# Kernel optimization log

Hardware: AMD Instinct MI355X
Metric: run time of the kernel (lower is better)

Reference implementation:

```python
import jax, jax.numpy as jnp
import numpy as np

N_NODES = 50000
N_GRAPHS = 128
HEADS = 10
F_XD = 78


def _linear(x, W, b):
    return x @ W + b


def _conv1d(x, w, b):
    # x: [B, Cin, L], w: [Cout, Cin, K]
    y = jax.lax.conv_general_dilated(x, w, (1,), 'VALID',
                                     dimension_numbers=('NCH', 'OIH', 'NCH'))
    return y + b[None, :, None]


def _add_self_loops(src, dst, n):
    loop = jnp.arange(n, dtype=src.dtype)
    return jnp.concatenate([src, loop]), jnp.concatenate([dst, loop])


def _gat_conv(x, src, dst, W, att_src, att_dst, b, n):
    # PyG GATConv, concat heads, self-loops, negative_slope=0.2
    h = (x @ W).reshape(n, HEADS, F_XD)               # [N,H,F]
    a_s = jnp.sum(h * att_src[None], axis=-1)          # [N,H]
    a_d = jnp.sum(h * att_dst[None], axis=-1)          # [N,H]
    e = jax.nn.leaky_relu(a_s[src] + a_d[dst], 0.2)    # [E,H]
    m = jax.ops.segment_max(e, dst, num_segments=n)    # [N,H]
    m = jnp.where(jnp.isfinite(m), m, 0.0)
    ex = jnp.exp(e - m[dst])
    s = jax.ops.segment_sum(ex, dst, num_segments=n)
    alpha = ex / (s[dst] + 1e-16)                      # [E,H]
    out = jax.ops.segment_sum(h[src] * alpha[:, :, None], dst, num_segments=n)
    return out.reshape(n, HEADS * F_XD) + b


def _gcn_conv(x, src, dst, W, b, n):
    # PyG GCNConv: self-loops + symmetric normalization
    h = x @ W                                          # [N,C]
    ones = jnp.ones(src.shape[0], dtype=h.dtype)
    deg = jax.ops.segment_sum(ones, dst, num_segments=n)
    dinv = jnp.where(deg > 0, jax.lax.rsqrt(deg), 0.0)
    norm = dinv[src] * dinv[dst]                       # [E]
    out = jax.ops.segment_sum(h[src] * norm[:, None], dst, num_segments=n)
    return out + b


def _forward(x, edge_index, batch, target1, target2, params):
    p = params
    n = x.shape[0]
    src0, dst0 = edge_index[0], edge_index[1]
    src, dst = _add_self_loops(src0, dst0, n)

    h = jax.nn.relu(_gat_conv(x, src, dst, p['W_gat'], p['att_src'], p['att_dst'], p['b_gat'], n))
    h = jax.nn.relu(_gcn_conv(h, src, dst, p['W_gcn'], p['b_gcn'], n))

    # global max + mean pool per graph
    cnt = jax.ops.segment_sum(jnp.ones(n, dtype=h.dtype), batch, num_segments=N_GRAPHS)
    gmx = jax.ops.segment_max(h, batch, num_segments=N_GRAPHS)
    gmx = jnp.where(cnt[:, None] > 0, gmx, 0.0)
    gav = jax.ops.segment_sum(h, batch, num_segments=N_GRAPHS) / jnp.maximum(cnt, 1.0)[:, None]
    g = jnp.concatenate([gmx, gav], axis=1)            # [B,1560]

    g = jax.nn.relu(_linear(g, p['W_fcg1'], p['b_fcg1']))  # dropout = identity (eval)
    g = _linear(g, p['W_fcg2'], p['b_fcg2'])               # [B,128]

    # protein branch 2: embedding + conv1d over embed dim
    emb = p['emb'][target2]                            # [B,1000,128]
    xt2 = _conv1d(emb, p['Wc2'], p['bc2'])             # [B,32,121]
    xt2 = _linear(xt2.reshape(xt2.shape[0], 32 * 121), p['W_fc2xt'], p['b_fc2xt'])

    # protein branch 1: conv1d on raw float features
    xt1 = _conv1d(target1, p['Wc1'], p['bc1'])         # [B,32,17]
    xt1 = _linear(xt1.reshape(xt1.shape[0], 544), p['W_fc1xt'], p['b_fc1xt'])

    xc = jnp.concatenate([g, xt1, xt2], axis=1)        # [B,384]
    xc = jax.nn.relu(_linear(xc, p['W_fc1'], p['b_fc1']))
    xc = jax.nn.relu(_linear(xc, p['W_fc2'], p['b_fc2']))
    return _linear(xc, p['W_out'], p['b_out'])         # [B,1]


def setup_inputs() -> dict:
    key = jax.random.key(0)
    ks = jax.random.split(key, 32)

    def w(k, shape, fan_in):
        return jax.random.normal(k, shape, dtype=jnp.float32) * (1.0 / np.sqrt(fan_in))

    inp = {}
    inp['x'] = jax.random.normal(ks[0], (N_NODES, F_XD), dtype=jnp.float32)
    inp['edge_index'] = jax.random.randint(ks[1], (2, 150000), 0, N_NODES, dtype=jnp.int64) if jax.config.jax_enable_x64 else jax.random.randint(ks[1], (2, 150000), 0, N_NODES).astype(jnp.int32)
    inp['batch'] = jnp.sort(jax.random.randint(ks[2], (N_NODES,), 0, N_GRAPHS)).astype(jnp.int32)
    inp['target1'] = jax.random.normal(ks[3], (N_GRAPHS, 20, 24), dtype=jnp.float32)
    inp['target2'] = jax.random.randint(ks[4], (N_GRAPHS, 1000), 0, 26).astype(jnp.int32)

    inp['W_gat'] = w(ks[5], (F_XD, HEADS * F_XD), F_XD)
    inp['att_src'] = w(ks[6], (HEADS, F_XD), F_XD)
    inp['att_dst'] = w(ks[7], (HEADS, F_XD), F_XD)
    inp['b_gat'] = jnp.zeros((HEADS * F_XD,), jnp.float32)
    inp['W_gcn'] = w(ks[8], (780, 780), 780)
    inp['b_gcn'] = jnp.zeros((780,), jnp.float32)
    inp['W_fcg1'] = w(ks[9], (1560, 1500), 1560)
    inp['b_fcg1'] = jnp.zeros((1500,), jnp.float32)
    inp['W_fcg2'] = w(ks[10], (1500, 128), 1500)
    inp['b_fcg2'] = jnp.zeros((128,), jnp.float32)
    inp['emb'] = jax.random.normal(ks[11], (26, 128), dtype=jnp.float32)
    inp['Wc2'] = w(ks[12], (32, 1000, 8), 1000 * 8)
    inp['bc2'] = jnp.zeros((32,), jnp.float32)
    inp['W_fc2xt'] = w(ks[13], (32 * 121, 128), 32 * 121)
    inp['b_fc2xt'] = jnp.zeros((128,), jnp.float32)
    inp['Wc1'] = w(ks[14], (32, 20, 8), 20 * 8)
    inp['bc1'] = jnp.zeros((32,), jnp.float32)
    inp['W_fc1xt'] = w(ks[15], (544, 128), 544)
    inp['b_fc1xt'] = jnp.zeros((128,), jnp.float32)
    inp['W_fc1'] = w(ks[16], (384, 1024), 384)
    inp['b_fc1'] = jnp.zeros((1024,), jnp.float32)
    inp['W_fc2'] = w(ks[17], (1024, 512), 1024)
    inp['b_fc2'] = jnp.zeros((512,), jnp.float32)
    inp['W_out'] = w(ks[18], (512, 1), 512)
    inp['b_out'] = jnp.zeros((1,), jnp.float32)
    return inp


def reference(x, edge_index, batch, target1, target2,
              W_gat, att_src, att_dst, b_gat, W_gcn, b_gcn,
              W_fcg1, b_fcg1, W_fcg2, b_fcg2, emb, Wc2, bc2,
              W_fc2xt, b_fc2xt, Wc1, bc1, W_fc1xt, b_fc1xt,
              W_fc1, b_fc1, W_fc2, b_fc2, W_out, b_out):
    params = dict(W_gat=W_gat, att_src=att_src, att_dst=att_dst, b_gat=b_gat,
                  W_gcn=W_gcn, b_gcn=b_gcn, W_fcg1=W_fcg1, b_fcg1=b_fcg1,
                  W_fcg2=W_fcg2, b_fcg2=b_fcg2, emb=emb, Wc2=Wc2, bc2=bc2,
                  W_fc2xt=W_fc2xt, b_fc2xt=b_fc2xt, Wc1=Wc1, bc1=bc1,
                  W_fc1xt=W_fc1xt, b_fc1xt=b_fc1xt, W_fc1=W_fc1, b_fc1=b_fc1,
                  W_fc2=W_fc2, b_fc2=b_fc2, W_out=W_out, b_out=b_out)
    return _forward(x, edge_index, batch, target1, target2, params)
```

## Files before the change

kernel.cpp:

```cpp
#include <hip/hip_runtime.h>
#include <cstdio>
#include <cstdint>

#define CDIV(a,b) (((a)+(b)-1)/(b))

static const int N   = 50000;
static const int NE0 = 150000;
static const int NE  = 200000;
static const int H   = 10;
static const int F   = 78;
static const int C   = 780;
static const int G   = 128;
static const int KP_GAT = 96;
static const int XAGG_LD = 960;
static const int CP1 = 800;
static const int CP1A = 832;
static const int CP2 = 784;
static const int POOL_SPLIT = 8;
static const int BM_SPLIT = 4;

typedef __attribute__((ext_vector_type(8))) short bf16x8;
typedef __attribute__((ext_vector_type(4))) float f32x4;
typedef __attribute__((ext_vector_type(8))) unsigned short us8;

__device__ __forceinline__ float bf2f(unsigned short u) {
    return __uint_as_float(((unsigned int)u) << 16);
}
__device__ __forceinline__ unsigned short f2bf(float f) {
    unsigned int u = __float_as_uint(f);
    u = (u + 0x7fff + ((u >> 16) & 1)) >> 16;
    return (unsigned short)u;
}

__device__ __forceinline__ void async16(const unsigned short* g, unsigned short* l) {
    __builtin_amdgcn_global_load_lds(
        (const __attribute__((address_space(1))) unsigned int*)g,
        (__attribute__((address_space(3))) unsigned int*)l, 16, 0, 0);
}

__global__ __launch_bounds__(512)
void gemm_mfma_256(const unsigned short* __restrict__ A,
                   const unsigned short* __restrict__ Bt,
                   unsigned short* __restrict__ Cb,
                   const float* __restrict__ bias, int relu,
                   int M, int Nn, int kSteps, int lda, int ldb, int ldc, int nct)
{
    __shared__ unsigned short As[256][64];
    __shared__ unsigned short Bs[128][64];
    const int tid  = threadIdx.x;
    const int lane = tid & 63;
    const int wave = tid >> 6;
    const int wm = (wave >> 1) * 64;
    const int wn = (wave & 1) * 64;

    const int nwg = gridDim.x;
    const int q8 = nwg >> 3, r8 = nwg & 7;
    const int xcd = blockIdx.x & 7, sub = blockIdx.x >> 3;
    const int wg = (xcd < r8) ? xcd * (q8 + 1) + sub
                              : r8 * (q8 + 1) + (xcd - r8) * q8 + sub;
    const int bm = (wg / nct) * 256, bn = (wg % nct) * 128;

    f32x4 acc[4][4] = {};

    const int mrow = lane & 15, quad = lane >> 4;
    const int srow = lane >> 3;
    const int segoff = ((lane & 7) ^ (lane >> 3)) * 8;

    const unsigned short* gA[4];
    unsigned short* lA[4];
#pragma unroll
    for (int c = 0; c < 4; c++) {
        int r = c * 64 + wave * 8 + srow;
        gA[c] = A + (size_t)min(bm + r, M - 1) * lda + segoff;
        lA[c] = &As[c * 64 + wave * 8][0];
    }
    const unsigned short* gB[2];
    unsigned short* lB[2];
#pragma unroll
    for (int c = 0; c < 2; c++) {
        int r = c * 64 + wave * 8 + srow;
        gB[c] = Bt + (size_t)min(bn + r, Nn - 1) * ldb + segoff;
        lB[c] = &Bs[c * 64 + wave * 8][0];
    }

    for (int ks = 0; ks < kSteps; ks++) {
        const int k0 = ks * 64;
#pragma unroll
        for (int c = 0; c < 4; c++) async16(gA[c] + k0, lA[c]);
#pragma unroll
        for (int c = 0; c < 2; c++) async16(gB[c] + k0, lB[c]);
        __syncthreads();
#pragma unroll
        for (int kk = 0; kk < 2; kk++) {
            bf16x8 af[4], bfr[4];
#pragma unroll
            for (int i = 0; i < 4; i++) {
                int ra = wm + i * 16 + mrow;
                af[i]  = *(const bf16x8*)&As[ra][(((kk * 4 + quad) ^ (ra & 7))) * 8];
                int rb = wn + i * 16 + mrow;
                bfr[i] = *(const bf16x8*)&Bs[rb][(((kk * 4 + quad) ^ (rb & 7))) * 8];
            }
#pragma unroll
            for (int i = 0; i < 4; i++)
#pragma unroll
                for (int j = 0; j < 4; j++)
                    acc[i][j] = __builtin_amdgcn_mfma_f32_16x16x32_bf16(af[i], bfr[j], acc[i][j], 0, 0, 0);
        }
        __syncthreads();
    }

#pragma unroll
    for (int i = 0; i < 4; i++) {
#pragma unroll
        for (int j = 0; j < 4; j++) {
            int col = bn + wn + j * 16 + mrow;
            if (col >= Nn) continue;
            float bv = bias ? bias[col] : 0.f;
#pragma unroll
            for (int r = 0; r < 4; r++) {
                int row = bm + wm + i * 16 + quad * 4 + r;
                if (row >= M) continue;
                float v = acc[i][j][r] + bv;
                if (relu) v = fmaxf(v, 0.f);
                Cb[(size_t)row * ldc + col] = f2bf(v);
            }
        }
    }
}

__global__ __launch_bounds__(256)
void gemm_gat(const unsigned short* __restrict__ A,
              const unsigned short* __restrict__ Bt,
              const float* __restrict__ bias,
              unsigned short* __restrict__ Cb)
{
    __shared__ unsigned short As[128][32];
    __shared__ unsigned short Bs[128][32];
    const int tid  = threadIdx.x;
    const int lane = tid & 63;
    const int wave = tid >> 6;
    const int wm = (wave >> 1) * 64, wn = (wave & 1) * 64;
    const int h = blockIdx.y;

    const int nwg = gridDim.x;
    const int q8 = nwg >> 3, r8 = nwg & 7;
    const int xcd = blockIdx.x & 7, sub = blockIdx.x >> 3;
    const int wg = (xcd < r8) ? xcd * (q8 + 1) + sub
                              : r8 * (q8 + 1) + (xcd - r8) * q8 + sub;
    const int bm = wg * 128;

    f32x4 acc[4][4] = {};

    const int mrow = lane & 15, quad = lane >> 4;
    const int subr = lane >> 2;
    const int segp = ((lane & 3) ^ ((lane >> 3) & 3)) * 8;
    const int segr = (quad ^ ((mrow >> 1) & 3)) * 8;

    const unsigned short* gA0 = A + (size_t)min(bm + wave * 16 + subr,      N - 1) * XAGG_LD + h * KP_GAT + segp;
    const unsigned short* gA1 = A + (size_t)min(bm + 64 + wave * 16 + subr, N - 1) * XAGG_LD + h * KP_GAT + segp;
    const unsigned short* gB0 = Bt + (size_t)(h * 80 + min(wave * 16 + subr,      79)) * KP_GAT + segp;
    const unsigned short* gB1 = Bt + (size_t)(h * 80 + min(64 + wave * 16 + subr, 79)) * KP_GAT + segp;
    unsigned short* lA0 = &As[wave * 16][0];
    unsigned short* lA1 = &As[64 + wave * 16][0];
    unsigned short* lB0 = &Bs[wave * 16][0];
    unsigned short* lB1 = &Bs[64 + wave * 16][0];

#pragma unroll
    for (int ks = 0; ks < 3; ks++) {
        const int k0 = ks * 32;
        async16(gA0 + k0, lA0);
        async16(gA1 + k0, lA1);
        async16(gB0 + k0, lB0);
        async16(gB1 + k0, lB1);
        __syncthreads();
        bf16x8 af[4], bfr[4];
#pragma unroll
        for (int i = 0; i < 4; i++) {
            af[i]  = *(const bf16x8*)&As[wm + i * 16 + mrow][segr];
            bfr[i] = *(const bf16x8*)&Bs[wn + i * 16 + mrow][segr];
        }
#pragma unroll
        for (int i = 0; i < 4; i++)
#pragma unroll
            for (int j = 0; j < 4; j++)
                acc[i][j] = __builtin_amdgcn_mfma_f32_16x16x32_bf16(af[i], bfr[j], acc[i][j], 0, 0, 0);
        __syncthreads();
    }

#pragma unroll
    for (int i = 0; i < 4; i++) {
#pragma unroll
        for (int j = 0; j < 4; j++) {
            int cl = wn + j * 16 + mrow;
            if (cl >= 80) continue;
            float bv = bias[h * 80 + cl];
#pragma unroll
            for (int r = 0; r < 4; r++) {
                int row = bm + wm + i * 16 + quad * 4 + r;
                if (row >= N) continue;
                float v = fmaxf(acc[i][j][r] + bv, 0.f);
                Cb[(size_t)row * CP1A + h * 80 + cl] = f2bf(v);
            }
        }
    }
}

__global__ __launch_bounds__(256)
void gemm_mfma_sk(const unsigned short* __restrict__ A,
                  const unsigned short* __restrict__ Bt,
                  float* __restrict__ Cp,
                  int M, int Nn, int kSteps, int lda, int ldb, int nct)
{
    __shared__ unsigned short As[128][32];
    __shared__ unsigned short Bs[128][32];
    const int tid  = threadIdx.x;
    const int lane = tid & 63;
    const int wave = tid >> 6;
    const int wm = (wave >> 1) * 64, wn = (wave & 1) * 64;
    const int bm = (blockIdx.x / nct) * 128, bn = (blockIdx.x % nct) * 128;

    const int split = blockIdx.y, KS = gridDim.y;
    const int per = CDIV(kSteps, KS);
    const int kb = split * per;
    const int ke = min(kb + per, kSteps);

    f32x4 acc[4][4] = {};

    const int mrow = lane & 15, quad = lane >> 4;
    const int subr = lane >> 2;
    const int segp = ((lane & 3) ^ ((lane >> 3) & 3)) * 8;
    const int segr = (quad ^ ((mrow >> 1) & 3)) * 8;

    const unsigned short* gA0 = A  + (size_t)min(bm + wave * 16 + subr,      M - 1)  * lda + segp;
    const unsigned short* gA1 = A  + (size_t)min(bm + 64 + wave * 16 + subr, M - 1)  * lda + segp;
    const unsigned short* gB0 = Bt + (size_t)min(bn + wave * 16 + subr,      Nn - 1) * ldb + segp;
    const unsigned short* gB1 = Bt + (size_t)min(bn + 64 + wave * 16 + subr, Nn - 1) * ldb + segp;
    unsigned short* lA0 = &As[wave * 16][0];
    unsigned short* lA1 = &As[64 + wave * 16][0];
    unsigned short* lB0 = &Bs[wave * 16][0];
    unsigned short* lB1 = &Bs[64 + wave * 16][0];

    for (int ks = kb; ks < ke; ks++) {
        const int k0 = ks * 32;
        async16(gA0 + k0, lA0);
        async16(gA1 + k0, lA1);
        async16(gB0 + k0, lB0);
        async16(gB1 + k0, lB1);
        __syncthreads();
        bf16x8 af[4], bfr[4];
#pragma unroll
        for (int i = 0; i < 4; i++) {
            af[i]  = *(const bf16x8*)&As[wm + i * 16 + mrow][segr];
            bfr[i] = *(const bf16x8*)&Bs[wn + i * 16 + mrow][segr];
        }
#pragma unroll
        for (int i = 0; i < 4; i++)
#pragma unroll
            for (int j = 0; j < 4; j++)
                acc[i][j] = __builtin_amdgcn_mfma_f32_16x16x32_bf16(af[i], bfr[j], acc[i][j], 0, 0, 0);
        __syncthreads();
    }

    float* Cs = Cp + (size_t)split * M * Nn;
#pragma unroll
    for (int i = 0; i < 4; i++) {
#pragma unroll
        for (int j = 0; j < 4; j++) {
            int col = bn + wn + j * 16 + mrow;
            if (col >= Nn) continue;
#pragma unroll
            for (int r = 0; r < 4; r++) {
                int row = bm + wm + i * 16 + quad * 4 + r;
                if (row >= M) continue;
                Cs[(size_t)row * Nn + col] = acc[i][j][r];
            }
        }
    }
}

__global__ void k_sk_reduce(const float* __restrict__ Cp, int KS, int M, int Nn,
                            const float* __restrict__ bias, int relu,
                            unsigned short* __restrict__ Cb, int ldc)
{
    int idx = blockIdx.x * blockDim.x + threadIdx.x;
    if (idx >= M * Nn) return;
    int row = idx / Nn, col = idx % Nn;
    float v = bias ? bias[col] : 0.f;
    for (int s = 0; s < KS; s++) v += Cp[((size_t)s * M + row) * Nn + col];
    if (relu) v = fmaxf(v, 0.f);
    Cb[(size_t)row * ldc + col] = f2bf(v);
}

__global__ void k_fc_out(const unsigned short* __restrict__ f2, const float* __restrict__ W,
                         const float* __restrict__ b, float* __restrict__ out)
{
    int g = blockIdx.x, lane = threadIdx.x;
    float acc = 0.f;
    for (int k = lane; k < 512; k += 64) acc += bf2f(f2[g * 512 + k]) * W[k];
#pragma unroll
    for (int off = 32; off > 0; off >>= 1) acc += __shfl_down(acc, off, 64);
    if (lane == 0) out[g] = acc + b[0];
}

__global__ void k_cast_pad_x(const float* __restrict__ x, unsigned short* __restrict__ xb)
{
    int idx = blockIdx.x * blockDim.x + threadIdx.x;
    if (idx >= N * KP_GAT) return;
    int n = idx / KP_GAT, k = idx % KP_GAT;
    float v = (k < F) ? x[(size_t)n * F + k] : 0.f;
    xb[idx] = f2bf(v);
}

__global__ void k_transpose_cast_t(const float* __restrict__ W, unsigned short* __restrict__ Wt,
                                   int K, int Nn, int Kpad)
{
    __shared__ float tile[32][33];
    int k0 = blockIdx.x * 32, n0 = blockIdx.y * 32;
    int tx = threadIdx.x, ty = threadIdx.y;
    for (int r = ty; r < 32; r += 8) {
        int k = k0 + r, n = n0 + tx;
        tile[r][tx] = (k < K && n < Nn) ? W[(size_t)k * Nn + n] : 0.f;
    }
    __syncthreads();
    for (int r = ty; r < 32; r += 8) {
        int n = n0 + r, k = k0 + tx;
        if (n < Nn && k < Kpad) Wt[(size_t)n * Kpad + k] = f2bf(tile[tx][r]);
    }
}

__global__ void k_build_Wgat_t(const float* __restrict__ W_gat, unsigned short* __restrict__ Wt)
{
    int idx = blockIdx.x * blockDim.x + threadIdx.x;
    if (idx >= KP_GAT * CP1) return;
    int k = idx / CP1, n = idx % CP1;
    int h = n / 80, f = n % 80;
    float v = (k < F && f < F) ? W_gat[(size_t)k * C + h * F + f] : 0.f;
    Wt[(size_t)n * KP_GAT + k] = f2bf(v);
}

__global__ void k_build_bgat(const float* __restrict__ b_gat, float* __restrict__ bp)
{
    int i = blockIdx.x * blockDim.x + threadIdx.x;
    if (i >= CP1) return;
    int h = i / 80, f = i % 80;
    bp[i] = (f < F) ? b_gat[h * F + f] : 0.f;
}

__global__ void k_build_Wgcn_t(const float* __restrict__ W_gcn, unsigned short* __restrict__ Wt)
{
    int idx = blockIdx.x * blockDim.x + threadIdx.x;
    if (idx >= C * CP2) return;
    int ko = idx / CP2, n = idx % CP2;
    int h = ko / F, f = ko % F;
    float v = (n < C) ? W_gcn[(size_t)ko * C + n] : 0.f;
    Wt[(size_t)n * CP1A + h * 80 + f] = f2bf(v);
}

__global__ void k_Vsd(const float* __restrict__ W_gat, const float* __restrict__ att_src,
                      const float* __restrict__ att_dst, float* __restrict__ V_s,
                      float* __restrict__ V_d)
{
    int idx = blockIdx.x * blockDim.x + threadIdx.x;
    if (idx >= F * H) return;
    int k = idx / H, h = idx % H;
    const float* wr = W_gat + (size_t)k * C + h * F;
    const float* as = att_src + h * F;
    const float* ad = att_dst + h * F;
    float s = 0.f, d = 0.f;
    for (int f = 0; f < F; f++) { float w = wr[f]; s += w * as[f]; d += w * ad[f]; }
    V_s[idx] = s; V_d[idx] = d;
}

__global__ void k_ascores(const float* __restrict__ x, const float* __restrict__ V_s,
                          const float* __restrict__ V_d, float* __restrict__ a_s,
                          float* __restrict__ a_d)
{
    __shared__ float Vs[F * H], Vd[F * H];
    int t = threadIdx.x;
    for (int i = t; i < F * H; i += 256) { Vs[i] = V_s[i]; Vd[i] = V_d[i]; }
    __syncthreads();
    int n = blockIdx.x * 256 + t;
    if (n >= N) return;
    const float* xr = x + (size_t)n * F;
    float accs[H] = {}, accd[H] = {};
    for (int k = 0; k < F; k++) {
        float xv = xr[k];
        const float* vs = &Vs[k * H];
        const float* vd = &Vd[k * H];
#pragma unroll
        for (int h = 0; h < H; h++) { accs[h] += xv * vs[h]; accd[h] += xv * vd[h]; }
    }
    for (int h = 0; h < H; h++) { a_s[n * H + h] = accs[h]; a_d[n * H + h] = accd[h]; }
}

__global__ void count_deg(const int* __restrict__ ei, int* __restrict__ deg)
{
    int e = blockIdx.x * blockDim.x + threadIdx.x;
    if (e >= NE) return;
    int d = (e < NE0) ? ei[NE0 + e] : (e - NE0);
    atomicAdd(&deg[d], 1);
}

__global__ void scan_int(const int* __restrict__ cnt, int* __restrict__ row_start, int n)
{
    __shared__ int partial[1024];
    int tid = threadIdx.x;
    int per = CDIV(n, 1024);
    int start = tid * per, end = min(start + per, n);
    int sum = 0;
    for (int i = start; i < end; i++) sum += cnt[i];
    partial[tid] = sum;
    __syncthreads();
    for (int off = 1; off < 1024; off *= 2) {
        int v = (tid >= off) ? partial[tid - off] : 0;
        __syncthreads();
        partial[tid] += v;
        __syncthreads();
    }
    int base = (tid > 0) ? partial[tid - 1] : 0;
    for (int i = start; i < end; i++) { row_start[i] = base; base += cnt[i]; }
    if (tid == 1023) row_start[n] = base;
}

__global__ void fill_csr_ev(const int* __restrict__ ei, const int* __restrict__ row_start,
                            int* __restrict__ fill_cnt, int* __restrict__ srcs,
                            const float* __restrict__ a_s, const float* __restrict__ a_d,
                            float* __restrict__ evb)
{
    int e = blockIdx.x * blockDim.x + threadIdx.x;
    if (e >= NE) return;
    int sr = (e < NE0) ? ei[e] : (e - NE0);
    int d  = (e < NE0) ? ei[NE0 + e] : (e - NE0);
    int pos = row_start[d] + atomicAdd(&fill_cnt[d], 1);
    srcs[pos] = sr;
    const float* as = a_s + sr * H;
    const float* ad = a_d + d * H;
    float* ev = evb + (size_t)pos * H;
#pragma unroll
    for (int h = 0; h < H; h++) {
        float v = as[h] + ad[h];
        ev[h] = (v > 0.f) ? v : 0.2f * v;
    }
}

__global__ void k_gstart(const int* __restrict__ batch, int* __restrict__ gstart)
{
    int g = blockIdx.x * blockDim.x + threadIdx.x;
    if (g > G) return;
    int lo = 0, hi = N;
    while (lo < hi) {
        int mid = (lo + hi) >> 1;
        if (batch[mid] < g) lo = mid + 1; else hi = mid;
    }
    gstart[g] = lo;
}

__global__ void k_softmax_alpha(const int* __restrict__ row_start, float* __restrict__ evb)
{
    int idx = blockIdx.x * blockDim.x + threadIdx.x;
    if (idx >= N * H) return;
    int n = idx / H, h = idx % H;
    int rs = row_start[n], re = row_start[n + 1];
    float m = -INFINITY, s = 0.f;
    for (int i = rs; i < re; i++) {
        float ev = evb[(size_t)i * H + h];
        if (ev <= m) {
            s += expf(ev - m);
        } else {
            s = s * expf(m - ev) + 1.f;
            m = ev;
        }
    }
    float inv = 1.f / (s + 1e-16f);
    for (int i = rs; i < re; i++) {
        float ev = evb[(size_t)i * H + h];
        evb[(size_t)i * H + h] = expf(ev - m) * inv;
    }
}

__global__ __launch_bounds__(128)
void gat_agg_x(const unsigned short* __restrict__ xb, const float* __restrict__ alpha,
               const int* __restrict__ srcs, const int* __restrict__ row_start,
               unsigned short* __restrict__ xagg)
{
    int n = blockIdx.x;
    int f = threadIdx.x;
    if (f >= KP_GAT) return;
    int rs = row_start[n], re = row_start[n + 1];
    float acc[H] = {};
    int i = rs;
    for (; i + 1 < re; i += 2) {
        int sr0 = srcs[i], sr1 = srcs[i + 1];
        float xv0 = bf2f(xb[(size_t)sr0 * KP_GAT + f]);
        float xv1 = bf2f(xb[(size_t)sr1 * KP_GAT + f]);
        const float* al0 = alpha + (size_t)i * H;
        const float* al1 = alpha + (size_t)(i + 1) * H;
#pragma unroll
        for (int h = 0; h < H; h++) acc[h] += al0[h] * xv0 + al1[h] * xv1;
    }
    if (i < re) {
        int sr = srcs[i];
        float xv = bf2f(xb[(size_t)sr * KP_GAT + f]);
        const float* al = alpha + (size_t)i * H;
#pragma unroll
        for (int h = 0; h < H; h++) acc[h] += al[h] * xv;
    }
#pragma unroll
    for (int h = 0; h < H; h++)
        xagg[(size_t)n * XAGG_LD + h * KP_GAT + f] = f2bf(acc[h]);
}

__global__ void k_zero_tail(unsigned short* __restrict__ gat_out)
{
    int idx = blockIdx.x * blockDim.x + threadIdx.x;
    if (idx >= N * 32) return;
    int n = idx / 32, c = idx % 32;
    gat_out[(size_t)n * CP1A + CP1 + c] = 0;
}

__global__ void k_dinv(const int* __restrict__ deg, float* __restrict__ dinv)
{
    int n = blockIdx.x * blockDim.x + threadIdx.x;
    if (n >= N) return;
    int d = deg[n];
    dinv[n] = (d > 0) ? 1.f / sqrtf((float)d) : 0.f;
}

__global__ __launch_bounds__(128)
void gcn_agg(const unsigned short* __restrict__ h2, const float* __restrict__ dinv,
             const int* __restrict__ srcs, const int* __restrict__ row_start,
             const float* __restrict__ b_gcn, unsigned short* __restrict__ out)
{
    int n = blockIdx.x;
    int c = threadIdx.x * 8;
    if (c >= CP2) return;
    float dn = dinv[n];
    int rs = row_start[n], re = row_start[n + 1];
    float acc[8] = {};
    int i = rs;
    for (; i + 1 < re; i += 2) {
        int sr0 = srcs[i], sr1 = srcs[i + 1];
        float d0 = dinv[sr0], d1 = dinv[sr1];
        us8 v0 = *(const us8*)&h2[(size_t)sr0 * CP2 + c];
        us8 v1 = *(const us8*)&h2[(size_t)sr1 * CP2 + c];
#pragma unroll
        for (int j = 0; j < 8; j++) acc[j] += d0 * bf2f(v0[j]) + d1 * bf2f(v1[j]);
    }
    if (i < re) {
        int sr = srcs[i];
        float d = dinv[sr];
        us8 v = *(const us8*)&h2[(size_t)sr * CP2 + c];
#pragma unroll
        for (int j = 0; j < 8; j++) acc[j] += d * bf2f(v[j]);
    }
    us8 o;
#pragma unroll
    for (int j = 0; j < 8; j++) {
        int col = c + j;
        float r = (col < C) ? fmaxf(acc[j] * dn + b_gcn[col], 0.f) : 0.f;
        o[j] = f2bf(r);
    }
    *(us8*)&out[(size_t)n * CP2 + c] = o;
}

__global__ __launch_bounds__(128)
void k_pool(const unsigned short* __restrict__ hh, const int* __restrict__ gstart,
            float* __restrict__ gfeat)
{
    int g = blockIdx.x;
    int c = threadIdx.x * 8;
    if (c >= CP2) return;
    int s0 = gstart[g], e0 = gstart[g + 1];
    int len = e0 - s0;
    if (len <= 0) return;
    int per = CDIV(len, (int)gridDim.y);
    int s = s0 + (int)blockIdx.y * per;
    int e = min(s + per, e0);
    if (s >= e) return;
    float mx[8] = {}, sm[8] = {};
    for (int n = s; n < e; n++) {
        us8 v = *(const us8*)&hh[(size_t)n * CP2 + c];
#pragma unroll
        for (int j = 0; j < 8; j++) { float f = bf2f(v[j]); mx[j] = fmaxf(mx[j], f); sm[j] += f; }
    }
#pragma unroll
    for (int j = 0; j < 8; j++) {
        int col = c + j;
        if (col < C) {
            atomicMax((unsigned int*)&gfeat[g * 1560 + col], __float_as_uint(mx[j]));
            atomicAdd(&gfeat[g * 1560 + 780 + col], sm[j]);
        }
    }
}

__global__ void k_pool_cast(const float* __restrict__ gfeat, const int* __restrict__ gstart,
                            unsigned short* __restrict__ dst)
{
    int idx = blockIdx.x * blockDim.x + threadIdx.x;
    if (idx >= G * 1568) return;
    int g = idx / 1568, k = idx % 1568;
    float v = 0.f;
    if (k < 780) {
        v = gfeat[g * 1560 + k];
    } else if (k < 1560) {
        float cnt = fmaxf((float)(gstart[g + 1] - gstart[g]), 1.f);
        v = gfeat[g * 1560 + k] * (1.f / cnt);
    }
    dst[idx] = f2bf(v);
}

__global__ void k_build_M(const int* __restrict__ t2, const float* __restrict__ Wc2,
                          float* __restrict__ Mbuf)
{
    __shared__ float Ml[26 * 256];
    int b = blockIdx.x, t = threadIdx.x, s = blockIdx.y;
    for (int j = t; j < 26 * 256; j += 256) Ml[j] = 0.f;
    __syncthreads();
    int o = t >> 3, k = t & 7;
    const int* tb = t2 + b * 1000;
    int c0 = s * (1000 / BM_SPLIT), c1 = c0 + (1000 / BM_SPLIT);
    for (int cc = c0; cc < c1; cc++) {
        int tok = tb[cc];
        Ml[tok * 256 + t] += Wc2[o * 8000 + cc * 8 + k];
    }
    __syncthreads();
    float* Mb = Mbuf + ((size_t)b * BM_SPLIT + s) * (26 * 256);
    for (int j = t; j < 26 * 256; j += 256) Mb[j] = Ml[j];
}

__global__ void k_reduce_M(const float* __restrict__ Mbuf, float* __restrict__ Mfin)
{
    int idx = blockIdx.x * blockDim.x + threadIdx.x;
    if (idx >= G * 26 * 256) return;
    int b = idx / (26 * 256), j = idx % (26 * 256);
    const float* p = Mbuf + (size_t)b * BM_SPLIT * (26 * 256);
    float v = 0.f;
#pragma unroll
    for (int s = 0; s < BM_SPLIT; s++) v += p[(size_t)s * (26 * 256) + j];
    Mfin[idx] = v;
}

__global__ void k_conv2(const float* __restrict__ Mbuf, const float* __restrict__ emb,
                        const float* __restrict__ bc2, unsigned short* __restrict__ xt2c)
{
    int idx = blockIdx.x * blockDim.x + threadIdx.x;
    if (idx >= G * 3872) return;
    int b = idx / 3872, r = idx % 3872;
    int o = r / 121, l = r % 121;
    const float* Mb = Mbuf + (size_t)b * (26 * 256);
    float acc = bc2[o];
    for (int t = 0; t < 26; t++) {
        const float* mrow = Mb + t * 256 + o * 8;
        const float* erow = emb + t * 128 + l;
#pragma unroll
        for (int k = 0; k < 8; k++) acc += mrow[k] * erow[k];
    }
    xt2c[idx] = f2bf(acc);
}

__global__ void k_conv1(const float* __restrict__ t1, const float* __restrict__ Wc1,
                        const float* __restrict__ bc1, unsigned short* __restrict__ xt1c)
{
    int idx = blockIdx.x * blockDim.x + threadIdx.x;
    if (idx >= G * 544) return;
    int b = idx / 544, r = idx % 544;
    int o = r / 17, l = r % 17;
    float acc = bc1[o];
    const float* xb = t1 + b * 480;
    const float* wo = Wc1 + o * 160;
    for (int cc = 0; cc < 20; cc++) {
        const float* xr = xb + cc * 24 + l;
        const float* wr = wo + cc * 8;
#pragma unroll
        for (int k = 0; k < 8; k++) acc += xr[k] * wr[k];
    }
    xt1c[idx] = f2bf(acc);
}

extern "C" void kernel_launch(void* const* d_in, const int* in_sizes, int n_in,
                              void* d_out, int out_size, void* d_ws, size_t ws_size,
                              hipStream_t stream)
{
    const float* x       = (const float*)d_in[0];
    const int*   ei      = (const int*)  d_in[1];
    const int*   batch   = (const int*)  d_in[2];
    const float* t1      = (const float*)d_in[3];
    const int*   t2      = (const int*)  d_in[4];
    const float* W_gat   = (const float*)d_in[5];
    const float* att_src = (const float*)d_in[6];
    const float* att_dst = (const float*)d_in[7];
    const float* b_gat   = (const float*)d_in[8];
    const float* W_gcn   = (const float*)d_in[9];
    const float* b_gcn   = (const float*)d_in[10];
    const float* W_fcg1  = (const float*)d_in[11];
    const float* b_fcg1  = (const float*)d_in[12];
    const float* W_fcg2  = (const float*)d_in[13];
    const float* b_fcg2  = (const float*)d_in[14];
    const float* emb     = (const float*)d_in[15];
    const float* Wc2     = (const float*)d_in[16];
    const float* bc2     = (const float*)d_in[17];
    const float* W_fc2xt = (const float*)d_in[18];
    const float* b_fc2xt = (const float*)d_in[19];
    const float* Wc1     = (const float*)d_in[20];
    const float* bc1     = (const float*)d_in[21];
    const float* W_fc1xt = (const float*)d_in[22];
    const float* b_fc1xt = (const float*)d_in[23];
    const float* W_fc1   = (const float*)d_in[24];
    const float* b_fc1   = (const float*)d_in[25];
    const float* W_fc2   = (const float*)d_in[26];
    const float* b_fc2   = (const float*)d_in[27];
    const float* W_out   = (const float*)d_in[28];
    const float* b_out   = (const float*)d_in[29];

    char* wsb = (char*)d_ws;
    size_t off = 0;
    auto alloc = [&](size_t bytes) -> char* {
        char* p = wsb + off;
        off += (bytes + 255) & ~(size_t)255;
        return p;
    };

    unsigned short* h_buf   = (unsigned short*)alloc((size_t)N * XAGG_LD * 2);
    unsigned short* gat_out = (unsigned short*)alloc((size_t)N * CP1A * 2);
    unsigned short* xb      = (unsigned short*)alloc((size_t)N * KP_GAT * 2);
    unsigned short* Wgat_t  = (unsigned short*)alloc((size_t)CP1 * KP_GAT * 2);
    unsigned short* Wgcn_t  = (unsigned short*)alloc((size_t)CP2 * CP1A * 2);
    unsigned short* Wfcg1_t  = (unsigned short*)alloc((size_t)1500 * 1568 * 2);
    unsigned short* Wfcg2_t  = (unsigned short*)alloc((size_t)128 * 1504 * 2);
    unsigned short* Wfc2xt_t = (unsigned short*)alloc((size_t)128 * 3872 * 2);
    unsigned short* Wfc1xt_t = (unsigned short*)alloc((size_t)128 * 544 * 2);
    unsigned short* Wfc1_t   = (unsigned short*)alloc((size_t)1024 * 384 * 2);
    unsigned short* Wfc2_t   = (unsigned short*)alloc((size_t)512 * 1024 * 2);
    unsigned short* gfeat_b  = (unsigned short*)alloc((size_t)G * 1568 * 2);
    unsigned short* g1_b     = (unsigned short*)alloc((size_t)G * 1504 * 2);
    unsigned short* xt2c_b   = (unsigned short*)alloc((size_t)G * 3872 * 2);
    unsigned short* xt1c_b   = (unsigned short*)alloc((size_t)G * 544 * 2);
    unsigned short* xc_b     = (unsigned short*)alloc((size_t)G * 384 * 2);
    unsigned short* f1_b     = (unsigned short*)alloc((size_t)G * 1024 * 2);
    unsigned short* f2_b     = (unsigned short*)alloc((size_t)G * 512 * 2);
    float* skbuf  = (float*)alloc((size_t)4 * G * 1500 * 4);
    float* bgat_p = (float*)alloc((size_t)CP1 * 4);
    float* V_s    = (float*)alloc((size_t)F * H * 4);
    float* V_d    = (float*)alloc((size_t)F * H * 4);
    float* a_s    = (float*)alloc((size_t)N * H * 4);
    float* a_d    = (float*)alloc((size_t)N * H * 4);
    float* evb    = (float*)alloc((size_t)NE * H * 4);
    float* dinv   = (float*)alloc((size_t)N * 4);
    float* gfeat  = (float*)alloc((size_t)G * 1560 * 4);
    float* Mbuf   = (float*)alloc((size_t)G * BM_SPLIT * 26 * 256 * 4);
    float* Mfin   = (float*)alloc((size_t)G * 26 * 256 * 4);
    int* deg       = (int*)alloc((size_t)N * 4);
    int* row_start = (int*)alloc((size_t)(N + 1) * 4);
    int* fill_cnt  = (int*)alloc((size_t)N * 4);
    int* srcs      = (int*)alloc((size_t)NE * 4);
    int* gstart    = (int*)alloc((size_t)(G + 1) * 4);

    if (off > ws_size) {
        fprintf(stderr, "kernel_launch: workspace too small: need %zu have %zu\n", off, ws_size);
        return;
    }

    hipMemsetAsync(deg, 0, (size_t)N * 4, stream);
    hipMemsetAsync(fill_cnt, 0, (size_t)N * 4, stream);
    hipMemsetAsync(g1_b, 0, (size_t)G * 1504 * 2, stream);
    hipMemsetAsync(Wgcn_t, 0, (size_t)CP2 * CP1A * 2, stream);
    hipMemsetAsync(gfeat, 0, (size_t)G * 1560 * 4, stream);

    dim3 tb(32, 8);

    k_cast_pad_x<<<CDIV(N * KP_GAT, 256), 256, 0, stream>>>(x, xb);
    k_build_Wgat_t<<<CDIV(KP_GAT * CP1, 256), 256, 0, stream>>>(W_gat, Wgat_t);
    k_build_bgat<<<CDIV(CP1, 256), 256, 0, stream>>>(b_gat, bgat_p);
    k_build_Wgcn_t<<<CDIV(C * CP2, 256), 256, 0, stream>>>(W_gcn, Wgcn_t);
    k_transpose_cast_t<<<dim3(CDIV(1568,32), CDIV(1500,32)), tb, 0, stream>>>(W_fcg1, Wfcg1_t, 1560, 1500, 1568);
    k_transpose_cast_t<<<dim3(CDIV(1504,32), CDIV(128,32)),  tb, 0, stream>>>(W_fcg2, Wfcg2_t, 1500, 128, 1504);
    k_transpose_cast_t<<<dim3(CDIV(3872,32), CDIV(128,32)),  tb, 0, stream>>>(W_fc2xt, Wfc2xt_t, 3872, 128, 3872);
    k_transpose_cast_t<<<dim3(CDIV(544,32),  CDIV(128,32)),  tb, 0, stream>>>(W_fc1xt, Wfc1xt_t, 544, 128, 544);
    k_transpose_cast_t<<<dim3(CDIV(384,32),  CDIV(1024,32)), tb, 0, stream>>>(W_fc1, Wfc1_t, 384, 1024, 384);
    k_transpose_cast_t<<<dim3(CDIV(1024,32), CDIV(512,32)),  tb, 0, stream>>>(W_fc2, Wfc2_t, 1024, 512, 1024);

    k_Vsd<<<CDIV(F * H, 256), 256, 0, stream>>>(W_gat, att_src, att_dst, V_s, V_d);
    k_ascores<<<CDIV(N, 256), 256, 0, stream>>>(x, V_s, V_d, a_s, a_d);

    count_deg<<<CDIV(NE, 256), 256, 0, stream>>>(ei, deg);
    scan_int<<<1, 1024, 0, stream>>>(deg, row_start, N);
    fill_csr_ev<<<CDIV(NE, 256), 256, 0, stream>>>(ei, row_start, fill_cnt, srcs, a_s, a_d, evb);
    k_gstart<<<1, 256, 0, stream>>>(batch, gstart);

    k_softmax_alpha<<<CDIV(N * H, 256), 256, 0, stream>>>(row_start, evb);
    k_dinv<<<CDIV(N, 256), 256, 0, stream>>>(deg, dinv);

    gat_agg_x<<<N, 128, 0, stream>>>(xb, evb, srcs, row_start, h_buf);
    gemm_gat<<<dim3(CDIV(N, 128), H), 256, 0, stream>>>(h_buf, Wgat_t, bgat_p, gat_out);
    k_zero_tail<<<CDIV(N * 32, 256), 256, 0, stream>>>(gat_out);

    {
        int rt = CDIV(N, 256), nct = CDIV(CP2, 128);
        gemm_mfma_256<<<rt * nct, 512, 0, stream>>>(gat_out, Wgcn_t, h_buf, nullptr, 0,
                                                    N, CP2, CP1A / 64, CP1A, CP1A, CP2, nct);
    }
    unsigned short* gcn_out = gat_out;
    gcn_agg<<<N, 128, 0, stream>>>(h_buf, dinv, srcs, row_start, b_gcn, gcn_out);
    k_pool<<<dim3(G, POOL_SPLIT), 128, 0, stream>>>(gcn_out, gstart, gfeat);
    k_pool_cast<<<CDIV(G * 1568, 256), 256, 0, stream>>>(gfeat, gstart, gfeat_b);

    gemm_mfma_sk<<<dim3(CDIV(1500,128), 4), 256, 0, stream>>>(gfeat_b, Wfcg1_t, skbuf,
                                                              G, 1500, 1568/32, 1568, 1568, CDIV(1500,128));
    k_sk_reduce<<<CDIV(G*1500, 256), 256, 0, stream>>>(skbuf, 4, G, 1500, b_fcg1, 1, g1_b, 1504);
    gemm_mfma_sk<<<dim3(1, 8), 256, 0, stream>>>(g1_b, Wfcg2_t, skbuf,
                                                 G, 128, 1504/32, 1504, 1504, 1);
    k_sk_reduce<<<CDIV(G*128, 256), 256, 0, stream>>>(skbuf, 8, G, 128, b_fcg2, 0, xc_b, 384);

    k_build_M<<<dim3(G, BM_SPLIT), 256, 0, stream>>>(t2, Wc2, Mbuf);
    k_reduce_M<<<CDIV(G * 26 * 256, 256), 256, 0, stream>>>(Mbuf, Mfin);
    k_conv2<<<CDIV(G * 3872, 256), 256, 0, stream>>>(Mfin, emb, bc2, xt2c_b);
    gemm_mfma_sk<<<dim3(1, 16), 256, 0, stream>>>(xt2c_b, Wfc2xt_t, skbuf,
                                                  G, 128, 3872/32, 3872, 3872, 1);
    k_sk_reduce<<<CDIV(G*128, 256), 256, 0, stream>>>(skbuf, 16, G, 128, b_fc2xt, 0, xc_b + 256, 384);

    k_conv1<<<CDIV(G * 544, 256), 256, 0, stream>>>(t1, Wc1, bc1, xt1c_b);
    gemm_mfma_sk<<<dim3(1, 4), 256, 0, stream>>>(xt1c_b, Wfc1xt_t, skbuf,
                                                 G, 128, 544/32, 544, 544, 1);
    k_sk_reduce<<<CDIV(G*128, 256), 256, 0, stream>>>(skbuf, 4, G, 128, b_fc1xt, 0, xc_b + 128, 384);

    gemm_mfma_sk<<<dim3(CDIV(1024,128), 4), 256, 0, stream>>>(xc_b, Wfc1_t, skbuf,
                                                              G, 1024, 384/32, 384, 384, CDIV(1024,128));
    k_sk_reduce<<<CDIV(G*1024, 256), 256, 0, stream>>>(skbuf, 4, G, 1024, b_fc1, 1, f1_b, 1024);
    gemm_mfma_sk<<<dim3(CDIV(512,128), 8), 256, 0, stream>>>(f1_b, Wfc2_t, skbuf,
                                                             G, 512, 1024/32, 1024, 1024, CDIV(512,128));
    k_sk_reduce<<<CDIV(G*512, 256), 256, 0, stream>>>(skbuf, 8, G, 512, b_fc2, 1, f2_b, 512);
    k_fc_out<<<G, 64, 0, stream>>>(f2_b, W_out, b_out, (float*)d_out);
}
```

Measured before the change: 657.1 us.

## Merge three small branch GEMMs into one block-diagonal GEMM and enlarge GAT tile

The three small per-branch GEMMs (fcg2, fc2xt, fc1xt) become a single split-K GEMM. Their activations are written into one concatenated buffer, and the transposed weights are packed into a zero-padded block-diagonal matrix. This removes several launches and split-K reductions, at the cost of multiplying zero blocks and building the packed weight every call. The conv branch kernels are launched earlier in the stream. gemm_gat now uses 256-row tiles with 512 threads so the B tile is reused across more rows, and BM_SPLIT is doubled.

```diff
diff --git a/kernel.cpp b/kernel.cpp
--- a/kernel.cpp
+++ b/kernel.cpp
@@ -17,7 +17,8 @@
 static const int CP1A = 832;
 static const int CP2 = 784;
 static const int POOL_SPLIT = 8;
-static const int BM_SPLIT = 4;
+static const int BM_SPLIT = 8;
+static const int KCAT = 5920;
 
 typedef __attribute__((ext_vector_type(8))) short bf16x8;
 typedef __attribute__((ext_vector_type(4))) float f32x4;
@@ -128,18 +129,19 @@
     }
 }
 
-__global__ __launch_bounds__(256)
+__global__ __launch_bounds__(512)
 void gemm_gat(const unsigned short* __restrict__ A,
               const unsigned short* __restrict__ Bt,
               const float* __restrict__ bias,
               unsigned short* __restrict__ Cb)
 {
-    __shared__ unsigned short As[128][32];
+    __shared__ unsigned short As[256][32];
     __shared__ unsigned short Bs[128][32];
     const int tid  = threadIdx.x;
     const int lane = tid & 63;
     const int wave = tid >> 6;
-    const int wm = (wave >> 1) * 64, wn = (wave & 1) * 64;
+    const int wm = (wave >> 1) * 64;
+    const int wn = (wave & 1) * 64;
     const int h = blockIdx.y;
 
     const int nwg = gridDim.x;
@@ -147,7 +149,7 @@
     const int xcd = blockIdx.x & 7, sub = blockIdx.x >> 3;
     const int wg = (xcd < r8) ? xcd * (q8 + 1) + sub
                               : r8 * (q8 + 1) + (xcd - r8) * q8 + sub;
-    const int bm = wg * 128;
+    const int bm = wg * 256;
 
     f32x4 acc[4][4] = {};
 
@@ -156,14 +158,12 @@
     const int segp = ((lane & 3) ^ ((lane >> 3) & 3)) * 8;
     const int segr = (quad ^ ((mrow >> 1) & 3)) * 8;
 
-    const unsigned short* gA0 = A + (size_t)min(bm + wave * 16 + subr,      N - 1) * XAGG_LD + h * KP_GAT + segp;
-    const unsigned short* gA1 = A + (size_t)min(bm + 64 + wave * 16 + subr, N - 1) * XAGG_LD + h * KP_GAT + segp;
-    const unsigned short* gB0 = Bt + (size_t)(h * 80 + min(wave * 16 + subr,      79)) * KP_GAT + segp;
-    const unsigned short* gB1 = Bt + (size_t)(h * 80 + min(64 + wave * 16 + subr, 79)) * KP_GAT + segp;
+    const unsigned short* gA0 = A + (size_t)min(bm + wave * 16 + subr,       N - 1) * XAGG_LD + h * KP_GAT + segp;
+    const unsigned short* gA1 = A + (size_t)min(bm + 128 + wave * 16 + subr, N - 1) * XAGG_LD + h * KP_GAT + segp;
+    const unsigned short* gB0 = Bt + (size_t)(h * 80 + min(wave * 16 + subr, 79)) * KP_GAT + segp;
     unsigned short* lA0 = &As[wave * 16][0];
-    unsigned short* lA1 = &As[64 + wave * 16][0];
+    unsigned short* lA1 = &As[128 + wave * 16][0];
     unsigned short* lB0 = &Bs[wave * 16][0];
-    unsigned short* lB1 = &Bs[64 + wave * 16][0];
 
 #pragma unroll
     for (int ks = 0; ks < 3; ks++) {
@@ -171,7 +171,6 @@
         async16(gA0 + k0, lA0);
         async16(gA1 + k0, lA1);
         async16(gB0 + k0, lB0);
-        async16(gB1 + k0, lB1);
         __syncthreads();
         bf16x8 af[4], bfr[4];
 #pragma unroll
@@ -354,6 +353,33 @@
     int h = ko / F, f = ko % F;
     float v = (n < C) ? W_gcn[(size_t)ko * C + n] : 0.f;
     Wt[(size_t)n * CP1A + h * 80 + f] = f2bf(v);
+}
+
+__global__ void k_build_Wcat(const unsigned short* __restrict__ Wfcg2_t,
+                             const unsigned short* __restrict__ Wfc2xt_t,
+                             const unsigned short* __restrict__ Wfc1xt_t,
+                             unsigned short* __restrict__ Wcat)
+{
+    int idx = blockIdx.x * blockDim.x + threadIdx.x;
+    if (idx >= 384 * KCAT) return;
+    int n = idx / KCAT, k = idx % KCAT;
+    unsigned short v = 0;
+    if (n < 128) {
+        if (k < 1504) v = Wfcg2_t[(size_t)n * 1504 + k];
+    } else if (n < 256) {
+        if (k >= 5376) v = Wfc1xt_t[(size_t)(n - 128) * 544 + (k - 5376)];
+    } else {
+        if (k >= 1504 && k < 5376) v = Wfc2xt_t[(size_t)(n - 256) * 3872 + (k - 1504)];
+    }
+    Wcat[idx] = v;
+}
+
+__global__ void k_build_bcat(const float* __restrict__ b_fcg2, const float* __restrict__ b_fc1xt,
+                             const float* __restrict__ b_fc2xt, float* __restrict__ bcat)
+{
+    int i = threadIdx.x;
+    if (i >= 384) return;
+    bcat[i] = (i < 128) ? b_fcg2[i] : ((i < 256) ? b_fc1xt[i - 128] : b_fc2xt[i - 256]);
 }
 
 __global__ void k_Vsd(const float* __restrict__ W_gat, const float* __restrict__ att_src,
@@ -641,7 +667,7 @@
 }
 
 __global__ void k_conv2(const float* __restrict__ Mbuf, const float* __restrict__ emb,
-                        const float* __restrict__ bc2, unsigned short* __restrict__ xt2c)
+                        const float* __restrict__ bc2, unsigned short* __restrict__ dst, int ld)
 {
     int idx = blockIdx.x * blockDim.x + threadIdx.x;
     if (idx >= G * 3872) return;
@@ -655,11 +681,11 @@
 #pragma unroll
         for (int k = 0; k < 8; k++) acc += mrow[k] * erow[k];
     }
-    xt2c[idx] = f2bf(acc);
+    dst[(size_t)b * ld + r] = f2bf(acc);
 }
 
 __global__ void k_conv1(const float* __restrict__ t1, const float* __restrict__ Wc1,
-                        const float* __restrict__ bc1, unsigned short* __restrict__ xt1c)
+                        const float* __restrict__ bc1, unsigned short* __restrict__ dst, int ld)
 {
     int idx = blockIdx.x * blockDim.x + threadIdx.x;
     if (idx >= G * 544) return;
@@ -674,7 +700,7 @@
 #pragma unroll
         for (int k = 0; k < 8; k++) acc += xr[k] * wr[k];
     }
-    xt1c[idx] = f2bf(acc);
+    dst[(size_t)b * ld + r] = f2bf(acc);
 }
 
 extern "C" void kernel_launch(void* const* d_in, const int* in_sizes, int n_in,
@@ -731,15 +757,15 @@
     unsigned short* Wfc1xt_t = (unsigned short*)alloc((size_t)128 * 544 * 2);
     unsigned short* Wfc1_t   = (unsigned short*)alloc((size_t)1024 * 384 * 2);
     unsigned short* Wfc2_t   = (unsigned short*)alloc((size_t)512 * 1024 * 2);
+    unsigned short* Wcat     = (unsigned short*)alloc((size_t)384 * KCAT * 2);
+    unsigned short* Acat     = (unsigned short*)alloc((size_t)G * KCAT * 2);
     unsigned short* gfeat_b  = (unsigned short*)alloc((size_t)G * 1568 * 2);
-    unsigned short* g1_b     = (unsigned short*)alloc((size_t)G * 1504 * 2);
-    unsigned short* xt2c_b   = (unsigned short*)alloc((size_t)G * 3872 * 2);
-    unsigned short* xt1c_b   = (unsigned short*)alloc((size_t)G * 544 * 2);
     unsigned short* xc_b     = (unsigned short*)alloc((size_t)G * 384 * 2);
     unsigned short* f1_b     = (unsigned short*)alloc((size_t)G * 1024 * 2);
     unsigned short* f2_b     = (unsigned short*)alloc((size_t)G * 512 * 2);
-    float* skbuf  = (float*)alloc((size_t)4 * G * 1500 * 4);
+    float* skbuf  = (float*)alloc((size_t)16 * G * 384 * 4);
     float* bgat_p = (float*)alloc((size_t)CP1 * 4);
+    float* bcat   = (float*)alloc((size_t)384 * 4);
     float* V_s    = (float*)alloc((size_t)F * H * 4);
     float* V_d    = (float*)alloc((size_t)F * H * 4);
     float* a_s    = (float*)alloc((size_t)N * H * 4);
@@ -762,7 +788,7 @@
 
     hipMemsetAsync(deg, 0, (size_t)N * 4, stream);
     hipMemsetAsync(fill_cnt, 0, (size_t)N * 4, stream);
-    hipMemsetAsync(g1_b, 0, (size_t)G * 1504 * 2, stream);
+    hipMemsetAsync(Acat, 0, (size_t)G * KCAT * 2, stream);
     hipMemsetAsync(Wgcn_t, 0, (size_t)CP2 * CP1A * 2, stream);
     hipMemsetAsync(gfeat, 0, (size_t)G * 1560 * 4, stream);
 
@@ -778,6 +804,8 @@
     k_transpose_cast_t<<<dim3(CDIV(544,32),  CDIV(128,32)),  tb, 0, stream>>>(W_fc1xt, Wfc1xt_t, 544, 128, 544);
     k_transpose_cast_t<<<dim3(CDIV(384,32),  CDIV(1024,32)), tb, 0, stream>>>(W_fc1, Wfc1_t, 384, 1024, 384);
     k_transpose_cast_t<<<dim3(CDIV(1024,32), CDIV(512,32)),  tb, 0, stream>>>(W_fc2, Wfc2_t, 1024, 512, 1024);
+    k_build_Wcat<<<CDIV(384 * KCAT, 256), 256, 0, stream>>>(Wfcg2_t, Wfc2xt_t, Wfc1xt_t, Wcat);
+    k_build_bcat<<<1, 384, 0, stream>>>(b_fcg2, b_fc1xt, b_fc2xt, bcat);
 
     k_Vsd<<<CDIV(F * H, 256), 256, 0, stream>>>(W_gat, att_src, att_dst, V_s, V_d);
     k_ascores<<<CDIV(N, 256), 256, 0, stream>>>(x, V_s, V_d, a_s, a_d);
@@ -790,8 +818,13 @@
     k_softmax_alpha<<<CDIV(N * H, 256), 256, 0, stream>>>(row_start, evb);
     k_dinv<<<CDIV(N, 256), 256, 0, stream>>>(deg, dinv);
 
+    k_build_M<<<dim3(G, BM_SPLIT), 256, 0, stream>>>(t2, Wc2, Mbuf);
+    k_reduce_M<<<CDIV(G * 26 * 256, 256), 256, 0, stream>>>(Mbuf, Mfin);
+    k_conv2<<<CDIV(G * 3872, 256), 256, 0, stream>>>(Mfin, emb, bc2, Acat + 1504, KCAT);
+    k_conv1<<<CDIV(G * 544, 256), 256, 0, stream>>>(t1, Wc1, bc1, Acat + 5376, KCAT);
+
     gat_agg_x<<<N, 128, 0, stream>>>(xb, evb, srcs, row_start, h_buf);
-    gemm_gat<<<dim3(CDIV(N, 128), H), 256, 0, stream>>>(h_buf, Wgat_t, bgat_p, gat_out);
+    gemm_gat<<<dim3(CDIV(N, 256), H), 512, 0, stream>>>(h_buf, Wgat_t, bgat_p, gat_out);
     k_zero_tail<<<CDIV(N * 32, 256), 256, 0, stream>>>(gat_out);
 
     {
@@ -806,22 +839,11 @@
 
     gemm_mfma_sk<<<dim3(CDIV(1500,128), 4), 256, 0, stream>>>(gfeat_b, Wfcg1_t, skbuf,
                                                               G, 1500, 1568/32, 1568, 1568, CDIV(1500,128));
-    k_sk_reduce<<<CDIV(G*1500, 256), 256, 0, stream>>>(skbuf, 4, G, 1500, b_fcg1, 1, g1_b, 1504);
-    gemm_mfma_sk<<<dim3(1, 8), 256, 0, stream>>>(g1_b, Wfcg2_t, skbuf,
-                                                 G, 128, 1504/32, 1504, 1504, 1);
-    k_sk_reduce<<<CDIV(G*128, 256), 256, 0, stream>>>(skbuf, 8, G, 128, b_fcg2, 0, xc_b, 384);
-
-    k_build_M<<<dim3(G, BM_SPLIT), 256, 0, stream>>>(t2, Wc2, Mbuf);
-    k_reduce_M<<<CDIV(G * 26 * 256, 256), 256, 0, stream>>>(Mbuf, Mfin);
-    k_conv2<<<CDIV(G * 3872, 256), 256, 0, stream>>>(Mfin, emb, bc2, xt2c_b);
-    gemm_mfma_sk<<<dim3(1, 16), 256, 0, stream>>>(xt2c_b, Wfc2xt_t, skbuf,
-                                                  G, 128, 3872/32, 3872, 3872, 1);
-    k_sk_reduce<<<CDIV(G*128, 256), 256, 0, stream>>>(skbuf, 16, G, 128, b_fc2xt, 0, xc_b + 256, 384);
-
-    k_conv1<<<CDIV(G * 544, 256), 256, 0, stream>>>(t1, Wc1, bc1, xt1c_b);
-    gemm_mfma_sk<<<dim3(1, 4), 256, 0, stream>>>(xt1c_b, Wfc1xt_t, skbuf,
-                                                 G, 128, 544/32, 544, 544, 1);
-    k_sk_reduce<<<CDIV(G*128, 256), 256, 0, stream>>>(skbuf, 4, G, 128, b_fc1xt, 0, xc_b + 128, 384);
+    k_sk_reduce<<<CDIV(G*1500, 256), 256, 0, stream>>>(skbuf, 4, G, 1500, b_fcg1, 1, Acat, KCAT);
+
+    gemm_mfma_sk<<<dim3(3, 16), 256, 0, stream>>>(Acat, Wcat, skbuf,
+                                                  G, 384, KCAT/32, KCAT, KCAT, 3);
+    k_sk_reduce<<<CDIV(G*384, 256), 256, 0, stream>>>(skbuf, 16, G, 384, bcat, 0, xc_b, 384);
 
     gemm_mfma_sk<<<dim3(CDIV(1024,128), 4), 256, 0, stream>>>(xc_b, Wfc1_t, skbuf,
                                                               G, 1024, 384/32, 384, 384, CDIV(1024,128));
```

Measured after the change: 658.6 us. No clear change (+0.2%).
